# Kernel optimization log

Measured on AMD Instinct MI355X. Metric: run time of the kernel, lower is better.

Reference implementation:

```python
import jax, jax.numpy as jnp
import numpy as np

N, DIN, D, H, L, S, E = 3072, 64, 128, 4, 2, 4, 49152
NEG = -2.0**32 + 1.0


def _layernorm(x, g, b, eps=1e-5):
    m = jnp.mean(x, axis=-1, keepdims=True)
    v = jnp.var(x, axis=-1, keepdims=True)
    return (x - m) * jax.lax.rsqrt(v + eps) * g + b


def setup_inputs() -> dict:
    key = jax.random.key(0)
    ks = jax.random.split(key, 24)
    w = lambda k, shp: (0.02 * jax.random.normal(k, shp)).astype(jnp.float32)
    inp = {
        "x": jax.random.normal(ks[0], (N, DIN), dtype=jnp.float32),
        "edge_index": jax.random.randint(ks[1], (2, E), 0, N, dtype=jnp.int64) if jax.config.jax_enable_x64 else jax.random.randint(ks[1], (2, E), 0, N).astype(jnp.int32),
        "shortest_path_len": jax.random.randint(ks[2], (N, N), 0, 11).astype(jnp.int32),
        "edge_feat": jax.random.normal(ks[3], (N, N, S), dtype=jnp.float32),
        # input projection
        "node_W": w(ks[4], (DIN, D)), "node_b": jnp.zeros((D,), jnp.float32),
        # centrality / spatial / edge encodings
        "deg_emb": w(ks[5], (N, D)),
        "sp_emb": w(ks[6], (11, 1)),
        "edge_W": w(ks[7], (S, S)), "edge_b": jnp.zeros((S,), jnp.float32),
        # per-layer stacked attention params
        "ln1_g": jnp.ones((L, D), jnp.float32), "ln1_b": jnp.zeros((L, D), jnp.float32),
        "Wq": w(ks[8], (L, H, D, D)), "bq": jnp.zeros((L, H, D), jnp.float32),
        "Wk": w(ks[9], (L, H, D, D)), "bk": jnp.zeros((L, H, D), jnp.float32),
        "Wv": w(ks[10], (L, H, D, D)), "bv": jnp.zeros((L, H, D), jnp.float32),
        "Wo": w(ks[11], (L, H * D, D)), "bo": jnp.zeros((L, D), jnp.float32),
        "ln2_g": jnp.ones((L, D), jnp.float32), "ln2_b": jnp.zeros((L, D), jnp.float32),
        "ff_W": w(ks[12], (L, D, D)), "ff_b": jnp.zeros((L, D), jnp.float32),
        # output projection
        "out_W": w(ks[13], (D, D)), "out_b": jnp.zeros((D,), jnp.float32),
    }
    return inp


def reference(x, edge_index, shortest_path_len, edge_feat,
              node_W, node_b, deg_emb, sp_emb, edge_W, edge_b,
              ln1_g, ln1_b, Wq, bq, Wk, bk, Wv, bv, Wo, bo,
              ln2_g, ln2_b, ff_W, ff_b, out_W, out_b):
    # padding mask from raw features
    mask_idx = (jnp.sum(x, axis=1) != 0).astype(x.dtype)            # [N]
    mask = mask_idx[:, None] * mask_idx[None, :]                    # [N,N]

    h = x @ node_W + node_b                                         # [N,D]
    # centrality: degree of edge destinations
    deg = jax.ops.segment_sum(jnp.ones((edge_index.shape[1],), jnp.int32),
                              edge_index[1], num_segments=N)        # [N]
    h = h + deg_emb[deg]

    spatial = sp_emb[shortest_path_len][..., 0]                     # [N,N]
    edge_m = (edge_feat @ edge_W + edge_b).mean(axis=-1)            # [N,N]
    bias = spatial + edge_m
    scale = 1.0 / jnp.sqrt(jnp.asarray(D, x.dtype))

    for l in range(L):
        x_ln = _layernorm(h, ln1_g[l], ln1_b[l])                    # [N,D]
        q = jnp.einsum('nd,hdk->hnk', x_ln, Wq[l]) + bq[l][:, None, :]
        k = jnp.einsum('nd,hdk->hnk', x_ln, Wk[l]) + bk[l][:, None, :]
        v = jnp.einsum('nd,hdk->hnk', x_ln, Wv[l]) + bv[l][:, None, :]
        a = jnp.einsum('hnk,hmk->hnm', q, k) * scale + bias[None]   # [H,N,N]
        a = jnp.where(mask[None] == 0, NEG, a)
        s = jax.nn.softmax(a, axis=-1)
        s = jnp.where(mask[None] == 0, 0.0, s)
        o = jnp.einsum('hnm,hmd->hnd', s, v)                        # [H,N,D]
        cat = jnp.transpose(o, (1, 0, 2)).reshape(N, H * D)         # [N,H*D]
        x_out = cat @ Wo[l] + bo[l] + h
        h = _layernorm(x_out, ln2_g[l], ln2_b[l]) @ ff_W[l] + ff_b[l] + x_out

    return h @ out_W + out_b
```

## Files before the change

### kernel.cpp

```cpp
#include <hip/hip_runtime.h>
#include <math.h>

static constexpr int N   = 3072;
static constexpr int DIN = 64;
static constexpr int D   = 128;
static constexpr int H   = 4;
static constexpr int E   = 49152;
#define NEGV  (-4294967295.0f)
#define SCALE (0.08838834764831845f)

typedef unsigned short u16;
typedef __attribute__((ext_vector_type(8))) short short8;
typedef __attribute__((ext_vector_type(4))) float f32x4;
typedef __attribute__((ext_vector_type(4))) unsigned short u16x4;

__device__ __forceinline__ u16 f2bf(float f){
  unsigned int u = __float_as_uint(f);
  u += 0x7fff + ((u >> 16) & 1);
  return (u16)(u >> 16);
}
__device__ __forceinline__ float bf2f(u16 u){
  return __uint_as_float(((unsigned int)u) << 16);
}

// ... 30 lines not shown
    a0 = fmaf(xu, nodeW[u*D + t],      a0);
    a1 = fmaf(xu, nodeW[u*D + t + 64], a1);
  }
  h[i*D + t]      = a0;
  h[i*D + t + 64] = a1;
  float s2 = a0 + a1, sq = a0*a0 + a1*a1;
  #pragma unroll
  for(int o=32;o;o>>=1){ s2 += __shfl_xor(s2, o); sq += __shfl_xor(sq, o); }
  float mean = s2*(1.0f/128.0f);
  float var  = sq*(1.0f/128.0f) - mean*mean;
  float inv  = rsqrtf(var + 1e-5f);
  xln[i*D + t]      = (a0 - mean)*inv*g1[t]      + b1[t];
  xln[i*D + t + 64] = (a1 - mean)*inv*g1[t + 64] + b1[t + 64];
}

__global__ void k_bias(const int* __restrict__ spl, const float* __restrict__ ef,
                       const float* __restrict__ spe, const float* __restrict__ eW,
                       const float* __restrict__ eb, const float* __restrict__ mask,
                       u16* __restrict__ biasm){
  int idx = blockIdx.x*blockDim.x + threadIdx.x;
  int i = idx / N, j = idx % N;
  float wm0 = (eW[0] + eW[1] + eW[2] + eW[3])  * 0.25f;
  float wm1 = (eW[4] + eW[5] + eW[6] + eW[7])  * 0.25f;
  float wm2 = (eW[8] + eW[9] + eW[10]+ eW[11]) * 0.25f;
  float wm3 = (eW[12]+ eW[13]+ eW[14]+ eW[15]) * 0.25f;
  float bm  = (eb[0] + eb[1] + eb[2] + eb[3])  * 0.25f;
  float4 e4 = reinterpret_cast<const float4*>(ef)[idx];
  float em = fmaf(e4.x, wm0, fmaf(e4.y, wm1, fmaf(e4.z, wm2, fmaf(e4.w, wm3, bm))));
  float b = spe[spl[idx]] + em;
  float mk = mask[i]*mask[j];
  biasm[idx] = f2bf((mk != 0.0f) ? b : NEGV);
}

__global__ __launch_bounds__(256) void k_wt_all(const float* __restrict__ Wq, const float* __restrict__ Wk,
    const float* __restrict__ Wv, const float* __restrict__ ffW, const float* __restrict__ outW,
    u16* __restrict__ wt_qkv, u16* __restrict__ wt_ff, u16* __restrict__ wt_out){
  __shared__ float t[32][33];
  const int z = blockIdx.y;
  const float* src; u16* dst;
  if(z < 24){
    int l = z/12, r = z%12;
    const float* W = (r>>2)==0 ? Wq : (r>>2)==1 ? Wk : Wv;
    src = W + (size_t)(l*4 + (r&3))*16384;
    dst = wt_qkv + (size_t)z*16384;
  } else if(z < 26){
    src = ffW + (size_t)(z-24)*16384; dst = wt_ff + (size_t)(z-24)*16384;
  } else { src = outW; dst = wt_out; }
  const int ki = blockIdx.x & 3, ni = blockIdx.x >> 2;
  const int tid = threadIdx.x;
  #pragma unroll
  for(int i=0;i<4;i++){
    int idx = tid + i*256, r = idx>>5, c = idx&31;
    t[r][c] = src[(size_t)(ki*32+r)*128 + ni*32 + c];
  }
  __syncthreads();
  #pragma unroll
  for(int i=0;i<4;i++){
    int idx = tid + i*256, r = idx>>5, c = idx&31;
    dst[(size_t)(ni*32+r)*128 + ki*32 + c] = f2bf(t[c][r]);
  }
}

__global__ __launch_bounds__(256) void k_wt_wo(const float* __restrict__ Wo, u16* __restrict__ wt_wo){
  __shared__ float t[32][33];
  const int l = blockIdx.y;
  const float* src = Wo + (size_t)l*65536;
  u16* dst = wt_wo + (size_t)l*65536;
  const int ki = blockIdx.x & 15, ni = blockIdx.x >> 4;
  const int tid = threadIdx.x;
  #pragma unroll
  for(int i=0;i<4;i++){
    int idx = tid + i*256, r = idx>>5, c = idx&31;
    t[r][c] = src[(size_t)(ki*32+r)*128 + ni*32 + c];
  }
  __syncthreads();
  #pragma unroll
  for(int i=0;i<4;i++){
    int idx = tid + i*256, r = idx>>5, c = idx&31;
    dst[(size_t)(ni*32+r)*512 + ki*32 + c] = f2bf(t[c][r]);
  }
}

template<int MODE>
__device__ __forceinline__ void mgemm_body(const float* __restrict__ A, const u16* __restrict__ Bt,
                                           const float* __restrict__ bias, void* __restrict__ Cv){
  __shared__ u16 As[64*128];
  __shared__ u16 Bs[128*128];
  const int tid = threadIdx.x, w = tid>>6, lane = tid&63;
  const int g4 = lane>>4, l16 = lane&15;
  const int m0 = blockIdx.x*64;
  const int srow = tid>>4, sch = tid&15;
  f32x4 acc[8];
  #pragma unroll
  for(int nt=0;nt<8;++nt) acc[nt] = (f32x4){0.f,0.f,0.f,0.f};
  #pragma unroll
  for(int it=0;it<4;++it){
    int row = it*16 + srow;
    const float4* ap = reinterpret_cast<const float4*>(A + (size_t)(m0+row)*128 + sch*8);
    float4 x0 = ap[0], x1 = ap[1];
    u16x4 p0, p1;
    p0.x=f2bf(x0.x); p0.y=f2bf(x0.y); p0.z=f2bf(x0.z); p0.w=f2bf(x0.w);
    p1.x=f2bf(x1.x); p1.y=f2bf(x1.y); p1.z=f2bf(x1.z); p1.w=f2bf(x1.w);
    u16* dst = &As[row*128 + ((sch ^ (row&15))*8)];
    *reinterpret_cast<u16x4*>(dst)     = p0;
    *reinterpret_cast<u16x4*>(dst + 4) = p1;
  }
  #pragma unroll
  for(int it=0;it<8;++it){
    int row = it*16 + srow;
    short8 b = *reinterpret_cast<const short8*>(Bt + (size_t)row*128 + sch*8);
    *reinterpret_cast<short8*>(&Bs[row*128 + ((sch ^ (row&15))*8)]) = b;
  }
  __syncthreads();
  __builtin_amdgcn_s_setprio(1);
  #pragma unroll
  for(int c=0;c<4;++c){
    short8 af = *reinterpret_cast<const short8*>(&As[(w*16+l16)*128 + (((c*4+g4) ^ l16)*8)]);
    #pragma unroll
    for(int nt=0;nt<8;++nt){
      short8 bf = *reinterpret_cast<const short8*>(&Bs[(nt*16+l16)*128 + (((c*4+g4) ^ l16)*8)]);
      acc[nt] = __builtin_amdgcn_mfma_f32_16x16x32_bf16(af, bf, acc[nt], 0, 0, 0);
    }
  }
  __builtin_amdgcn_s_setprio(0);
  const int mrow = m0 + w*16 + g4*4;
  if(MODE == 2){
    __syncthreads();
    u16* T = Bs;
    #pragma unroll
    for(int nt=0;nt<8;++nt){
      const int col = nt*16 + l16;
      float bi = bias[col];
      u16x4 t;
      t.x = f2bf(acc[nt][0] + bi); t.y = f2bf(acc[nt][1] + bi);
      t.z = f2bf(acc[nt][2] + bi); t.w = f2bf(acc[nt][3] + bi);
      *reinterpret_cast<u16x4*>(&T[col*68 + (w*16 + g4*4)]) = t;
    }
    __syncthreads();
    #pragma unroll
    for(int i=0;i<4;++i){
      int slot = tid + i*256;
      int col = slot >> 3, q = slot & 7;
      short8 v = *reinterpret_cast<const short8*>(&T[col*68 + q*8]);
      *reinterpret_cast<short8*>((u16*)Cv + (size_t)col*N + m0 + q*8) = v;
    }
  } else {
    #pragma unroll
    for(int nt=0;nt<8;++nt){
      const int col = nt*16 + l16;
      float bi = bias[col];
      #pragma unroll
      for(int rg=0;rg<4;++rg){
        float v = acc[nt][rg] + bi;
        if(MODE == 1) ((u16*)Cv)[(size_t)(mrow+rg)*128 + col] = f2bf(v);
        else          ((float*)Cv)[(size_t)(mrow+rg)*128 + col] = v;
      }
    }
  }
}

__global__ __launch_bounds__(256) void k_mqkv(const float* __restrict__ xln, const u16* __restrict__ wt_qkv,
    const float* __restrict__ bq, const float* __restrict__ bk, const float* __restrict__ bv,
    u16* __restrict__ q, u16* __restrict__ k, u16* __restrict__ vT, int l){
  const int z = blockIdx.y, which = z>>2, head = z&3;
  const u16* Bt = wt_qkv + (size_t)(l*12 + z)*16384;
  if(which == 0)      mgemm_body<1>(xln, Bt, bq + (l*H+head)*D, q  + (size_t)head*N*D);
  else if(which == 1) mgemm_body<1>(xln, Bt, bk + (l*H+head)*D, k  + (size_t)head*N*D);
  else                mgemm_body<2>(xln, Bt, bv + (l*H+head)*D, vT + (size_t)head*N*D);
}

__global__ __launch_bounds__(256) void k_mout(const float* __restrict__ h, const u16* __restrict__ wt_out,
    const float* __restrict__ outb, float* __restrict__ out){
  mgemm_body<0>(h, wt_out, outb, out);
}

template<int S>
__global__ __launch_bounds__(256) void k_mwo(const float* __restrict__ opart, const float* __restrict__ mpart,
    const float* __restrict__ lpart, const float* __restrict__ mask, const u16* __restrict__ wt,
    const float* __restrict__ bo, const float* __restrict__ hres,
    float* __restrict__ xout, float* __restrict__ xln,
    const float* __restrict__ g2, const float* __restrict__ b2){
  __shared__ u16 As[64*128];
  __shared__ u16 Bs[128*128];
  const int tid = threadIdx.x, w = tid>>6, lane = tid&63;
  const int g4 = lane>>4, l16 = lane&15;
  const int m0 = blockIdx.x*64;
  const int srow = tid>>4, sch = tid&15;
  f32x4 acc[8];
  #pragma unroll
  for(int nt=0;nt<8;++nt) acc[nt] = (f32x4){0.f,0.f,0.f,0.f};
  for(int k0 = 0; k0 < 512; k0 += 128){
    const int hh = k0 >> 7;
    __syncthreads();
    #pragma unroll
    for(int it=0;it<4;++it){
      int row = it*16 + srow;
      int grow = m0 + row;
      float w_[S]; float M = -INFINITY; float mv[S], lv[S];
      #pragma unroll
      for(int s=0;s<S;++s){
        mv[s] = mpart[(size_t)(s*H + hh)*N + grow];
        lv[s] = lpart[(size_t)(s*H + hh)*N + grow];
        M = fmaxf(M, mv[s]);
      }
      float denom = 0.f;
      #pragma unroll
      for(int s=0;s<S;++s){ w_[s] = __expf(mv[s] - M); denom = fmaf(lv[s], w_[s], denom); }
      float scale = mask[grow] / denom;
      const int d = sch*8;
      float4 v0 = make_float4(0,0,0,0), v1 = make_float4(0,0,0,0);
      #pragma unroll
      for(int s=0;s<S;++s){
        const float4* op = reinterpret_cast<const float4*>(
            opart + ((size_t)(s*H + hh)*N + grow)*D + d);
        float4 a = op[0], b = op[1];
        v0.x = fmaf(a.x, w_[s], v0.x); v0.y = fmaf(a.y, w_[s], v0.y);
        v0.z = fmaf(a.z, w_[s], v0.z); v0.w = fmaf(a.w, w_[s], v0.w);
        v1.x = fmaf(b.x, w_[s], v1.x); v1.y = fmaf(b.y, w_[s], v1.y);
        v1.z = fmaf(b.z, w_[s], v1.z); v1.w = fmaf(b.w, w_[s], v1.w);
      }
      u16x4 p0, p1;
      p0.x=f2bf(v0.x*scale); p0.y=f2bf(v0.y*scale); p0.z=f2bf(v0.z*scale); p0.w=f2bf(v0.w*scale);
      p1.x=f2bf(v1.x*scale); p1.y=f2bf(v1.y*scale); p1.z=f2bf(v1.z*scale); p1.w=f2bf(v1.w*scale);
      u16* dst = &As[row*128 + ((sch ^ (row&15))*8)];
      *reinterpret_cast<u16x4*>(dst)     = p0;
      *reinterpret_cast<u16x4*>(dst + 4) = p1;
    }
    #pragma unroll
    for(int it=0;it<8;++it){
      int row = it*16 + srow;
      short8 b = *reinterpret_cast<const short8*>(wt + (size_t)row*512 + k0 + sch*8);
      *reinterpret_cast<short8*>(&Bs[row*128 + ((sch ^ (row&15))*8)]) = b;
    }
    __syncthreads();
    __builtin_amdgcn_s_setprio(1);
    #pragma unroll
    for(int c=0;c<4;++c){
      short8 af = *reinterpret_cast<const short8*>(&As[(w*16+l16)*128 + (((c*4+g4) ^ l16)*8)]);
      #pragma unroll
      for(int nt=0;nt<8;++nt){
        short8 bf = *reinterpret_cast<const short8*>(&Bs[(nt*16+l16)*128 + (((c*4+g4) ^ l16)*8)]);
        acc[nt] = __builtin_amdgcn_mfma_f32_16x16x32_bf16(af, bf, acc[nt], 0, 0, 0);
      }
    }
    __builtin_amdgcn_s_setprio(0);
  }
  const int mrow = m0 + w*16 + g4*4;
  float s_[4] = {0,0,0,0}, q_[4] = {0,0,0,0};
  #pragma unroll
  for(int nt=0;nt<8;++nt){
    const int col = nt*16 + l16;
    float bi = bo[col];
    #pragma unroll
    for(int rg=0;rg<4;++rg){
      float v = acc[nt][rg] + bi + hres[(size_t)(mrow+rg)*128 + col];
      acc[nt][rg] = v;
      s_[rg] += v; q_[rg] = fmaf(v, v, q_[rg]);
    }
  }
  #pragma unroll
  for(int o=1;o<16;o<<=1){
    #pragma unroll
    for(int rg=0;rg<4;++rg){ s_[rg] += __shfl_xor(s_[rg], o); q_[rg] += __shfl_xor(q_[rg], o); }
  }
  float mean[4], inv[4];
  #pragma unroll
  for(int rg=0;rg<4;++rg){
    mean[rg] = s_[rg]*(1.0f/128.0f);
    float var = q_[rg]*(1.0f/128.0f) - mean[rg]*mean[rg];
    inv[rg] = rsqrtf(var + 1e-5f);
  }
  #pragma unroll
  for(int nt=0;nt<8;++nt){
    const int col = nt*16 + l16;
    float gg = g2[col], bb = b2[col];
    #pragma unroll
    for(int rg=0;rg<4;++rg){
      float v = acc[nt][rg];
      xout[(size_t)(mrow+rg)*128 + col] = v;
      xln [(size_t)(mrow+rg)*128 + col] = (v - mean[rg])*inv[rg]*gg + bb;
    }
  }
}

__global__ __launch_bounds__(256) void k_mff(const float* __restrict__ xlnin, const u16* __restrict__ wt,
    const float* __restrict__ ffb, const float* __restrict__ res, float* __restrict__ hout,
    float* __restrict__ xlnout, const float* __restrict__ g1n, const float* __restrict__ b1n,
    int write_ln){
  __shared__ u16 As[64*128];
  __shared__ u16 Bs[128*128];
  const int tid = threadIdx.x, w = tid>>6, lane = tid&63;
  const int g4 = lane>>4, l16 = lane&15;
  const int m0 = blockIdx.x*64;
  const int srow = tid>>4, sch = tid&15;
  f32x4 acc[8];
  #pragma unroll
  for(int nt=0;nt<8;++nt) acc[nt] = (f32x4){0.f,0.f,0.f,0.f};
  #pragma unroll
  for(int it=0;it<4;++it){
    int row = it*16 + srow;
    const float4* ap = reinterpret_cast<const float4*>(xlnin + (size_t)(m0+row)*128 + sch*8);
    float4 x0 = ap[0], x1 = ap[1];
    u16x4 p0, p1;
    p0.x=f2bf(x0.x); p0.y=f2bf(x0.y); p0.z=f2bf(x0.z); p0.w=f2bf(x0.w);
    p1.x=f2bf(x1.x); p1.y=f2bf(x1.y); p1.z=f2bf(x1.z); p1.w=f2bf(x1.w);
    u16* dst = &As[row*128 + ((sch ^ (row&15))*8)];
    *reinterpret_cast<u16x4*>(dst)     = p0;
    *reinterpret_cast<u16x4*>(dst + 4) = p1;
  }
  #pragma unroll
  for(int it=0;it<8;++it){
    int row = it*16 + srow;
    short8 b = *reinterpret_cast<const short8*>(wt + (size_t)row*128 + sch*8);
    *reinterpret_cast<short8*>(&Bs[row*128 + ((sch ^ (row&15))*8)]) = b;
  }
  __syncthreads();
  __builtin_amdgcn_s_setprio(1);
  #pragma unroll
  for(int c=0;c<4;++c){
    short8 af = *reinterpret_cast<const short8*>(&As[(w*16+l16)*128 + (((c*4+g4) ^ l16)*8)]);
    #pragma unroll
    for(int nt=0;nt<8;++nt){
      short8 bf = *reinterpret_cast<const short8*>(&Bs[(nt*16+l16)*128 + (((c*4+g4) ^ l16)*8)]);
      acc[nt] = __builtin_amdgcn_mfma_f32_16x16x32_bf16(af, bf, acc[nt], 0, 0, 0);
    }
  }
  __builtin_amdgcn_s_setprio(0);
  const int mrow = m0 + w*16 + g4*4;
  float s_[4] = {0,0,0,0}, q_[4] = {0,0,0,0};
  #pragma unroll
  for(int nt=0;nt<8;++nt){
    const int col = nt*16 + l16;
    float bi = ffb[col];
    #pragma unroll
    for(int rg=0;rg<4;++rg){
      float v = acc[nt][rg] + bi + res[(size_t)(mrow+rg)*128 + col];
      acc[nt][rg] = v;
      s_[rg] += v; q_[rg] = fmaf(v, v, q_[rg]);
    }
  }
  #pragma unroll
  for(int nt=0;nt<8;++nt){
    const int col = nt*16 + l16;
    #pragma unroll
    for(int rg=0;rg<4;++rg)
      hout[(size_t)(mrow+rg)*128 + col] = acc[nt][rg];
  }
  if(write_ln){
    #pragma unroll
    for(int o=1;o<16;o<<=1){
      #pragma unroll
      for(int rg=0;rg<4;++rg){ s_[rg] += __shfl_xor(s_[rg], o); q_[rg] += __shfl_xor(q_[rg], o); }
    }
    #pragma unroll
    for(int rg=0;rg<4;++rg){
      float mean = s_[rg]*(1.0f/128.0f);
      float var  = q_[rg]*(1.0f/128.0f) - mean*mean;
      float inv  = rsqrtf(var + 1e-5f);
      s_[rg] = mean; q_[rg] = inv;
    }
    #pragma unroll
    for(int nt=0;nt<8;++nt){
      const int col = nt*16 + l16;
      float gg = g1n[col], bb = b1n[col];
      #pragma unroll
      for(int rg=0;rg<4;++rg)
        xlnout[(size_t)(mrow+rg)*128 + col] = (acc[nt][rg] - s_[rg])*q_[rg]*gg + bb;
    }
  }
}

__global__ __launch_bounds__(256) void k_attn(const u16* __restrict__ q, const u16* __restrict__ k,
                     const u16* __restrict__ vT, const u16* __restrict__ biasm,
                     float* __restrict__ opart, float* __restrict__ mpart, float* __restrict__ lpart,
                     int kvlen){
  const int tid  = threadIdx.x;
  const int w    = tid >> 6;
  const int lane = tid & 63;
  const int g4 = lane >> 4, l16 = lane & 15;
  const int head = blockIdx.y, sp = blockIdx.z;
  const int r0 = blockIdx.x*64 + w*16;
  __shared__ u16 Ks[64*128];
  __shared__ u16 Vs[64*128];
  __shared__ u16 P[4][16][40];

  const u16* qbase = q + ((size_t)head*N + r0)*D;
  short8 qf[4];
  #pragma unroll
  for(int c=0;c<4;c++)
    qf[c] = *reinterpret_cast<const short8*>(qbase + l16*D + c*32 + g4*8);

  f32x4 o[8];
  #pragma unroll
  for(int dt=0;dt<8;dt++) o[dt] = (f32x4){0.f,0.f,0.f,0.f};
  float m = -INFINITY, lsum = 0.0f;

  const u16* kh   = k  + (size_t)head*N*D;
  const u16* vTh  = vT + (size_t)head*D*N;
  const u16* brow = biasm + (size_t)(r0 + l16)*N;
  const int kv0 = sp*kvlen;

  const int krow = tid >> 4, kch = tid & 15;
  const int vrow = tid >> 3, vch = tid & 7;

  for(int j0 = kv0; j0 < kv0 + kvlen; j0 += 64){
    short8 kreg[4], vreg[4];
    #pragma unroll
    for(int it=0; it<4; ++it)
      kreg[it] = *reinterpret_cast<const short8*>(kh + (size_t)(j0 + it*16 + krow)*D + kch*8);
    #pragma unroll
    for(int it=0; it<4; ++it)
      vreg[it] = *reinterpret_cast<const short8*>(vTh + (size_t)(it*32 + vrow)*N + j0 + vch*8);
    u16x4 bb[4];
    #pragma unroll
    for(int z=0; z<4; ++z)
      bb[z] = *reinterpret_cast<const u16x4*>(brow + j0 + z*16 + g4*4);

    __syncthreads();
    #pragma unroll
    for(int it=0; it<4; ++it){
      int row = it*16 + krow;
      *reinterpret_cast<short8*>(&Ks[row*128 + ((kch ^ (row&15))*8)]) = kreg[it];
    }
    #pragma unroll
    for(int it=0; it<4; ++it){
      int d = it*32 + vrow;
      int row = d & 63, ch = ((d>>6)<<3) | vch;
      *reinterpret_cast<short8*>(&Vs[row*128 + ((ch ^ (row&15))*8)]) = vreg[it];
    }
    __syncthreads();

    #pragma unroll
    for(int ks=0; ks<2; ++ks){
      short8 kf[8];
      const int rowA = ks*32 + l16, rowB = rowA + 16;
      #pragma unroll
      for(int c=0;c<4;c++){
        kf[c]   = *reinterpret_cast<const short8*>(&Ks[rowA*128 + (((c*4+g4) ^ l16)*8)]);
        kf[4+c] = *reinterpret_cast<const short8*>(&Ks[rowB*128 + (((c*4+g4) ^ l16)*8)]);
      }
      f32x4 sA = (f32x4){0.f,0.f,0.f,0.f}, sB = sA;
      __builtin_amdgcn_s_setprio(1);
      #pragma unroll
      for(int c=0;c<4;c++){
        sA = __builtin_amdgcn_mfma_f32_16x16x32_bf16(kf[c],   qf[c], sA, 0, 0, 0);
        sB = __builtin_amdgcn_mfma_f32_16x16x32_bf16(kf[4+c], qf[c], sB, 0, 0, 0);
      }
      __builtin_amdgcn_s_setprio(0);
      u16x4 bA = bb[2*ks], bB = bb[2*ks+1];
      sA[0] = fmaf(sA[0], SCALE, bf2f(bA.x)); sA[1] = fmaf(sA[1], SCALE, bf2f(bA.y));
      sA[2] = fmaf(sA[2], SCALE, bf2f(bA.z)); sA[3] = fmaf(sA[3], SCALE, bf2f(bA.w));
      sB[0] = fmaf(sB[0], SCALE, bf2f(bB.x)); sB[1] = fmaf(sB[1], SCALE, bf2f(bB.y));
      sB[2] = fmaf(sB[2], SCALE, bf2f(bB.z)); sB[3] = fmaf(sB[3], SCALE, bf2f(bB.w));
      float pmax = fmaxf(fmaxf(fmaxf(sA[0],sA[1]), fmaxf(sA[2],sA[3])),
                         fmaxf(fmaxf(sB[0],sB[1]), fmaxf(sB[2],sB[3])));
      pmax = fmaxf(pmax, __shfl_xor(pmax, 16));
      pmax = fmaxf(pmax, __shfl_xor(pmax, 32));
      if(!__all(pmax - m <= 8.0f)){
        float mnew = fmaxf(m, pmax);
        float corr = __expf(m - mnew);
        lsum *= corr;
        float c0 = __shfl(corr, (lane & 48) | (g4*4 + 0));
        float c1 = __shfl(corr, (lane & 48) | (g4*4 + 1));
        float c2 = __shfl(corr, (lane & 48) | (g4*4 + 2));
        float c3 = __shfl(corr, (lane & 48) | (g4*4 + 3));
        #pragma unroll
        for(int dt=0;dt<8;dt++){
          o[dt][0] *= c0; o[dt][1] *= c1; o[dt][2] *= c2; o[dt][3] *= c3;
        }
        m = mnew;
      }
      f32x4 pA, pB;
      #pragma unroll
      for(int rg=0;rg<4;rg++){ pA[rg] = __expf(sA[rg] - m); pB[rg] = __expf(sB[rg] - m); }
      float ps = (pA[0]+pA[1]) + (pA[2]+pA[3]) + ((pB[0]+pB[1]) + (pB[2]+pB[3]));
      ps += __shfl_xor(ps, 16);
      ps += __shfl_xor(ps, 32);
      lsum += ps;
      u16x4 wa, wb;
      wa.x = f2bf(pA[0]); wa.y = f2bf(pA[1]); wa.z = f2bf(pA[2]); wa.w = f2bf(pA[3]);
      wb.x = f2bf(pB[0]); wb.y = f2bf(pB[1]); wb.z = f2bf(pB[2]); wb.w = f2bf(pB[3]);
      *reinterpret_cast<u16x4*>(&P[w][l16][g4*4])      = wa;
      *reinterpret_cast<u16x4*>(&P[w][l16][16 + g4*4]) = wb;
      short8 pf = *reinterpret_cast<const short8*>(&P[w][l16][g4*8]);
      __builtin_amdgcn_s_setprio(1);
      #pragma unroll
      for(int dt=0;dt<8;dt++){
        int d = dt*16 + l16;
        int row = d & 63;
        int ch  = ((dt>>2)<<3) | (ks<<2) | g4;
        short8 vf = *reinterpret_cast<const short8*>(&Vs[row*128 + ((ch ^ l16)*8)]);
        o[dt] = __builtin_amdgcn_mfma_f32_16x16x32_bf16(pf, vf, o[dt], 0, 0, 0);
      }
      __builtin_amdgcn_s_setprio(0);
    }
  }

  float* ob = opart + ((size_t)((sp*H + head)*N) + r0)*D;
  #pragma unroll
  for(int dt=0;dt<8;dt++){
    #pragma unroll
    for(int rg=0;rg<4;rg++)
      ob[(size_t)(g4*4+rg)*D + dt*16 + l16] = o[dt][rg];
  }
  if(g4 == 0){
    mpart[(size_t)(sp*H + head)*N + r0 + l16] = m;
    lpart[(size_t)(sp*H + head)*N + r0 + l16] = lsum;
  }
}

extern "C" void kernel_launch(void* const* d_in, const int* in_sizes, int n_in,
                              void* d_out, int out_size, void* d_ws, size_t ws_size,
                              hipStream_t stream){
  const float* x      = (const float*)d_in[0];
  const int*   ei     = (const int*)  d_in[1];
  const int*   spl    = (const int*)  d_in[2];
  const float* ef     = (const float*)d_in[3];
  const float* nodeW  = (const float*)d_in[4];
  const float* nodeb  = (const float*)d_in[5];
  const float* degemb = (const float*)d_in[6];
  const float* spe    = (const float*)d_in[7];
  const float* eW     = (const float*)d_in[8];
  const float* eb     = (const float*)d_in[9];
  const float* ln1g   = (const float*)d_in[10];
  const float* ln1b   = (const float*)d_in[11];
  const float* Wq     = (const float*)d_in[12];
  const float* bq     = (const float*)d_in[13];
  const float* Wk     = (const float*)d_in[14];
  const float* bk     = (const float*)d_in[15];
  const float* Wv     = (const float*)d_in[16];
  const float* bv     = (const float*)d_in[17];
  const float* Wo     = (const float*)d_in[18];
  const float* bo     = (const float*)d_in[19];
  const float* ln2g   = (const float*)d_in[20];
  const float* ln2b   = (const float*)d_in[21];
  const float* ffW    = (const float*)d_in[22];
  const float* ffb    = (const float*)d_in[23];
  const float* outW   = (const float*)d_in[24];
  const float* outb   = (const float*)d_in[25];

  constexpr size_t WT_ELEMS = 24*16384 + 2*16384 + 16384 + 2*65536;
  auto needed = [](int s)->size_t{
    size_t fl = 8192 + 3*(size_t)N*D;
    size_t bf = 3*(size_t)H*N*D + (size_t)N*N;
    size_t pf = (size_t)s*H*N*D + 2*(size_t)s*H*N;
    return fl*4 + bf*2 + pf*4 + WT_ELEMS*2;
  };
  int S = 2;
  if(needed(4) <= ws_size) S = 4;

  float* ws   = (float*)d_ws;
  int*   deg  = (int*)ws;
  float* mask = ws + 4096;
  float* h    = ws + 8192;
  float* xln  = h    + N*D;
  float* xout = xln  + N*D;
  u16*   qb   = (u16*)(xout + N*D);
  u16*   kb   = qb + (size_t)H*N*D;
  u16*   vTb  = kb + (size_t)H*N*D;
  u16*   biasm= vTb + (size_t)H*N*D;
  float* opart= (float*)(biasm + (size_t)N*N);
  float* mpart= opart + (size_t)S*H*N*D;
  float* lpart= mpart + (size_t)S*H*N;
  u16*   wt_qkv = (u16*)(lpart + (size_t)S*H*N);
  u16*   wt_ff  = wt_qkv + 24*16384;
  u16*   wt_out = wt_ff  + 2*16384;
  u16*   wt_wo  = wt_out + 16384;

  k_wt_all<<<dim3(16, 27), 256, 0, stream>>>(Wq, Wk, Wv, ffW, outW, wt_qkv, wt_ff, wt_out);
  k_wt_wo<<<dim3(64, 2), 256, 0, stream>>>(Wo, wt_wo);
  k_zero_deg<<<(N+255)/256, 256, 0, stream>>>(deg);
  k_deg<<<(E+255)/256, 256, 0, stream>>>(ei, deg);
  k_h0<<<N, 64, 0, stream>>>(x, nodeW, nodeb, degemb, deg, ln1g, ln1b, mask, h, xln);
  k_bias<<<(N*N)/256, 256, 0, stream>>>(spl, ef, spe, eW, eb, mask, biasm);

  for(int l = 0; l < 2; ++l){
    k_mqkv<<<dim3(N/64, 12), 256, 0, stream>>>(xln, wt_qkv, bq, bk, bv, qb, kb, vTb, l);
    k_attn<<<dim3(N/64, H, S), 256, 0, stream>>>(qb, kb, vTb, biasm, opart, mpart, lpart, N/S);
    if(S == 4)
      k_mwo<4><<<N/64, 256, 0, stream>>>(opart, mpart, lpart, mask, wt_wo + (size_t)l*65536,
                                         bo + l*D, h, xout, xln, ln2g + l*D, ln2b + l*D);
    else
      k_mwo<2><<<N/64, 256, 0, stream>>>(opart, mpart, lpart, mask, wt_wo + (size_t)l*65536,
                                         bo + l*D, h, xout, xln, ln2g + l*D, ln2b + l*D);
    k_mff<<<N/64, 256, 0, stream>>>(xln, wt_ff + (size_t)l*16384, ffb + l*D, xout, h, xln,
                                    ln1g + (l==0 ? D : 0), ln1b + (l==0 ? D : 0), l==0 ? 1 : 0);
  }
  k_mout<<<N/64, 256, 0, stream>>>(h, wt_out, outb, (float*)d_out);
}
```

Before: 242.3 us.

## Process two query tiles per wave in attention and raise KV split to eight

```diff
diff --git a/kernel.cpp b/kernel.cpp
--- a/kernel.cpp
+++ b/kernel.cpp
@@ -433,25 +433,29 @@
   const int lane = tid & 63;
   const int g4 = lane >> 4, l16 = lane & 15;
   const int head = blockIdx.y, sp = blockIdx.z;
-  const int r0 = blockIdx.x*64 + w*16;
+  const int r0 = blockIdx.x*128 + w*32;
   __shared__ u16 Ks[64*128];
   __shared__ u16 Vs[64*128];
-  __shared__ u16 P[4][16][40];
+  __shared__ u16 P[4][2][16][40];
 
   const u16* qbase = q + ((size_t)head*N + r0)*D;
-  short8 qf[4];
-  #pragma unroll
-  for(int c=0;c<4;c++)
-    qf[c] = *reinterpret_cast<const short8*>(qbase + l16*D + c*32 + g4*8);
-
-  f32x4 o[8];
-  #pragma unroll
-  for(int dt=0;dt<8;dt++) o[dt] = (f32x4){0.f,0.f,0.f,0.f};
-  float m = -INFINITY, lsum = 0.0f;
+  short8 qf0[4], qf1[4];
+  #pragma unroll
+  for(int c=0;c<4;c++){
+    qf0[c] = *reinterpret_cast<const short8*>(qbase + l16*D + c*32 + g4*8);
+    qf1[c] = *reinterpret_cast<const short8*>(qbase + (16+l16)*D + c*32 + g4*8);
+  }
+
+  f32x4 o0[8], o1[8];
+  #pragma unroll
+  for(int dt=0;dt<8;dt++){ o0[dt] = (f32x4){0.f,0.f,0.f,0.f}; o1[dt] = o0[dt]; }
+  float m0v = -INFINITY, ls0 = 0.0f;
+  float m1v = -INFINITY, ls1 = 0.0f;
 
   const u16* kh   = k  + (size_t)head*N*D;
   const u16* vTh  = vT + (size_t)head*D*N;
-  const u16* brow = biasm + (size_t)(r0 + l16)*N;
+  const u16* brow0 = biasm + (size_t)(r0 + l16)*N;
+  const u16* brow1 = biasm + (size_t)(r0 + 16 + l16)*N;
   const int kv0 = sp*kvlen;
 
   const int krow = tid >> 4, kch = tid & 15;
@@ -465,10 +469,12 @@
     #pragma unroll
     for(int it=0; it<4; ++it)
       vreg[it] = *reinterpret_cast<const short8*>(vTh + (size_t)(it*32 + vrow)*N + j0 + vch*8);
-    u16x4 bb[4];
-    #pragma unroll
-    for(int z=0; z<4; ++z)
-      bb[z] = *reinterpret_cast<const u16x4*>(brow + j0 + z*16 + g4*4);
+    u16x4 bb0[4], bb1[4];
+    #pragma unroll
+    for(int z=0; z<4; ++z){
+      bb0[z] = *reinterpret_cast<const u16x4*>(brow0 + j0 + z*16 + g4*4);
+      bb1[z] = *reinterpret_cast<const u16x4*>(brow1 + j0 + z*16 + g4*4);
+    }
 
     __syncthreads();
     #pragma unroll
@@ -493,50 +499,72 @@
         kf[c]   = *reinterpret_cast<const short8*>(&Ks[rowA*128 + (((c*4+g4) ^ l16)*8)]);
         kf[4+c] = *reinterpret_cast<const short8*>(&Ks[rowB*128 + (((c*4+g4) ^ l16)*8)]);
       }
-      f32x4 sA = (f32x4){0.f,0.f,0.f,0.f}, sB = sA;
+      f32x4 sA0 = (f32x4){0.f,0.f,0.f,0.f}, sB0 = sA0, sA1 = sA0, sB1 = sA0;
       __builtin_amdgcn_s_setprio(1);
       #pragma unroll
       for(int c=0;c<4;c++){
-        sA = __builtin_amdgcn_mfma_f32_16x16x32_bf16(kf[c],   qf[c], sA, 0, 0, 0);
-        sB = __builtin_amdgcn_mfma_f32_16x16x32_bf16(kf[4+c], qf[c], sB, 0, 0, 0);
+        sA0 = __builtin_amdgcn_mfma_f32_16x16x32_bf16(kf[c],   qf0[c], sA0, 0, 0, 0);
+        sB0 = __builtin_amdgcn_mfma_f32_16x16x32_bf16(kf[4+c], qf0[c], sB0, 0, 0, 0);
+        sA1 = __builtin_amdgcn_mfma_f32_16x16x32_bf16(kf[c],   qf1[c], sA1, 0, 0, 0);
+        sB1 = __builtin_amdgcn_mfma_f32_16x16x32_bf16(kf[4+c], qf1[c], sB1, 0, 0, 0);
       }
       __builtin_amdgcn_s_setprio(0);
-      u16x4 bA = bb[2*ks], bB = bb[2*ks+1];
-      sA[0] = fmaf(sA[0], SCALE, bf2f(bA.x)); sA[1] = fmaf(sA[1], SCALE, bf2f(bA.y));
-      sA[2] = fmaf(sA[2], SCALE, bf2f(bA.z)); sA[3] = fmaf(sA[3], SCALE, bf2f(bA.w));
-      sB[0] = fmaf(sB[0], SCALE, bf2f(bB.x)); sB[1] = fmaf(sB[1], SCALE, bf2f(bB.y));
-      sB[2] = fmaf(sB[2], SCALE, bf2f(bB.z)); sB[3] = fmaf(sB[3], SCALE, bf2f(bB.w));
-      float pmax = fmaxf(fmaxf(fmaxf(sA[0],sA[1]), fmaxf(sA[2],sA[3])),
-                         fmaxf(fmaxf(sB[0],sB[1]), fmaxf(sB[2],sB[3])));
-      pmax = fmaxf(pmax, __shfl_xor(pmax, 16));
-      pmax = fmaxf(pmax, __shfl_xor(pmax, 32));
-      if(!__all(pmax - m <= 8.0f)){
-        float mnew = fmaxf(m, pmax);
-        float corr = __expf(m - mnew);
-        lsum *= corr;
-        float c0 = __shfl(corr, (lane & 48) | (g4*4 + 0));
-        float c1 = __shfl(corr, (lane & 48) | (g4*4 + 1));
-        float c2 = __shfl(corr, (lane & 48) | (g4*4 + 2));
-        float c3 = __shfl(corr, (lane & 48) | (g4*4 + 3));
+      {
+        u16x4 bA = bb0[2*ks], bB = bb0[2*ks+1];
+        sA0[0] = fmaf(sA0[0], SCALE, bf2f(bA.x)); sA0[1] = fmaf(sA0[1], SCALE, bf2f(bA.y));
+        sA0[2] = fmaf(sA0[2], SCALE, bf2f(bA.z)); sA0[3] = fmaf(sA0[3], SCALE, bf2f(bA.w));
+        sB0[0] = fmaf(sB0[0], SCALE, bf2f(bB.x)); sB0[1] = fmaf(sB0[1], SCALE, bf2f(bB.y));
+        sB0[2] = fmaf(sB0[2], SCALE, bf2f(bB.z)); sB0[3] = fmaf(sB0[3], SCALE, bf2f(bB.w));
+      }
+      {
+        u16x4 bA = bb1[2*ks], bB = bb1[2*ks+1];
+        sA1[0] = fmaf(sA1[0], SCALE, bf2f(bA.x)); sA1[1] = fmaf(sA1[1], SCALE, bf2f(bA.y));
+        sA1[2] = fmaf(sA1[2], SCALE, bf2f(bA.z)); sA1[3] = fmaf(sA1[3], SCALE, bf2f(bA.w));
+        sB1[0] = fmaf(sB1[0], SCALE, bf2f(bB.x)); sB1[1] = fmaf(sB1[1], SCALE, bf2f(bB.y));
+        sB1[2] = fmaf(sB1[2], SCALE, bf2f(bB.z)); sB1[3] = fmaf(sB1[3], SCALE, bf2f(bB.w));
+      }
+      float p0 = fmaxf(fmaxf(fmaxf(sA0[0],sA0[1]), fmaxf(sA0[2],sA0[3])),
+                       fmaxf(fmaxf(sB0[0],sB0[1]), fmaxf(sB0[2],sB0[3])));
+      float p1 = fmaxf(fmaxf(fmaxf(sA1[0],sA1[1]), fmaxf(sA1[2],sA1[3])),
+                       fmaxf(fmaxf(sB1[0],sB1[1]), fmaxf(sB1[2],sB1[3])));
+      p0 = fmaxf(p0, __shfl_xor(p0, 16)); p0 = fmaxf(p0, __shfl_xor(p0, 32));
+      p1 = fmaxf(p1, __shfl_xor(p1, 16)); p1 = fmaxf(p1, __shfl_xor(p1, 32));
+      float dm = fmaxf(p0 - m0v, p1 - m1v);
+      if(!__all(dm <= 8.0f)){
+        float mn0 = fmaxf(m0v, p0), mn1 = fmaxf(m1v, p1);
+        float cr0 = __expf(m0v - mn0), cr1 = __expf(m1v - mn1);
+        ls0 *= cr0; ls1 *= cr1;
         #pragma unroll
-        for(int dt=0;dt<8;dt++){
-          o[dt][0] *= c0; o[dt][1] *= c1; o[dt][2] *= c2; o[dt][3] *= c3;
+        for(int rg=0;rg<4;++rg){
+          float c0 = __shfl(cr0, (lane & 48) | (g4*4 + rg));
+          float c1 = __shfl(cr1, (lane & 48) | (g4*4 + rg));
+          #pragma unroll
+          for(int dt=0;dt<8;dt++){ o0[dt][rg] *= c0; o1[dt][rg] *= c1; }
         }
-        m = mnew;
-      }
-      f32x4 pA, pB;
-      #pragma unroll
-      for(int rg=0;rg<4;rg++){ pA[rg] = __expf(sA[rg] - m); pB[rg] = __expf(sB[rg] - m); }
-      float ps = (pA[0]+pA[1]) + (pA[2]+pA[3]) + ((pB[0]+pB[1]) + (pB[2]+pB[3]));
-      ps += __shfl_xor(ps, 16);
-      ps += __shfl_xor(ps, 32);
-      lsum += ps;
+        m0v = mn0; m1v = mn1;
+      }
+      f32x4 pA0, pB0, pA1, pB1;
+      #pragma unroll
+      for(int rg=0;rg<4;rg++){
+        pA0[rg] = __expf(sA0[rg] - m0v); pB0[rg] = __expf(sB0[rg] - m0v);
+        pA1[rg] = __expf(sA1[rg] - m1v); pB1[rg] = __expf(sB1[rg] - m1v);
+      }
+      float ps0 = (pA0[0]+pA0[1]) + (pA0[2]+pA0[3]) + ((pB0[0]+pB0[1]) + (pB0[2]+pB0[3]));
+      float ps1 = (pA1[0]+pA1[1]) + (pA1[2]+pA1[3]) + ((pB1[0]+pB1[1]) + (pB1[2]+pB1[3]));
+      ps0 += __shfl_xor(ps0, 16); ps0 += __shfl_xor(ps0, 32);
+      ps1 += __shfl_xor(ps1, 16); ps1 += __shfl_xor(ps1, 32);
+      ls0 += ps0; ls1 += ps1;
       u16x4 wa, wb;
-      wa.x = f2bf(pA[0]); wa.y = f2bf(pA[1]); wa.z = f2bf(pA[2]); wa.w = f2bf(pA[3]);
-      wb.x = f2bf(pB[0]); wb.y = f2bf(pB[1]); wb.z = f2bf(pB[2]); wb.w = f2bf(pB[3]);
-      *reinterpret_cast<u16x4*>(&P[w][l16][g4*4])      = wa;
-      *reinterpret_cast<u16x4*>(&P[w][l16][16 + g4*4]) = wb;
-      short8 pf = *reinterpret_cast<const short8*>(&P[w][l16][g4*8]);
+      wa.x = f2bf(pA0[0]); wa.y = f2bf(pA0[1]); wa.z = f2bf(pA0[2]); wa.w = f2bf(pA0[3]);
+      wb.x = f2bf(pB0[0]); wb.y = f2bf(pB0[1]); wb.z = f2bf(pB0[2]); wb.w = f2bf(pB0[3]);
+      *reinterpret_cast<u16x4*>(&P[w][0][l16][g4*4])      = wa;
+      *reinterpret_cast<u16x4*>(&P[w][0][l16][16 + g4*4]) = wb;
+      wa.x = f2bf(pA1[0]); wa.y = f2bf(pA1[1]); wa.z = f2bf(pA1[2]); wa.w = f2bf(pA1[3]);
+      wb.x = f2bf(pB1[0]); wb.y = f2bf(pB1[1]); wb.z = f2bf(pB1[2]); wb.w = f2bf(pB1[3]);
+      *reinterpret_cast<u16x4*>(&P[w][1][l16][g4*4])      = wa;
+      *reinterpret_cast<u16x4*>(&P[w][1][l16][16 + g4*4]) = wb;
+      short8 pf0 = *reinterpret_cast<const short8*>(&P[w][0][l16][g4*8]);
+      short8 pf1 = *reinterpret_cast<const short8*>(&P[w][1][l16][g4*8]);
       __builtin_amdgcn_s_setprio(1);
       #pragma unroll
       for(int dt=0;dt<8;dt++){
@@ -544,22 +572,28 @@
         int row = d & 63;
         int ch  = ((dt>>2)<<3) | (ks<<2) | g4;
         short8 vf = *reinterpret_cast<const short8*>(&Vs[row*128 + ((ch ^ l16)*8)]);
-        o[dt] = __builtin_amdgcn_mfma_f32_16x16x32_bf16(pf, vf, o[dt], 0, 0, 0);
+        o0[dt] = __builtin_amdgcn_mfma_f32_16x16x32_bf16(pf0, vf, o0[dt], 0, 0, 0);
+        o1[dt] = __builtin_amdgcn_mfma_f32_16x16x32_bf16(pf1, vf, o1[dt], 0, 0, 0);
       }
       __builtin_amdgcn_s_setprio(0);
     }
   }
 
-  float* ob = opart + ((size_t)((sp*H + head)*N) + r0)*D;
+  float* ob0 = opart + ((size_t)((sp*H + head)*N) + r0)*D;
+  float* ob1 = ob0 + (size_t)16*D;
   #pragma unroll
   for(int dt=0;dt<8;dt++){
     #pragma unroll
-    for(int rg=0;rg<4;rg++)
-      ob[(size_t)(g4*4+rg)*D + dt*16 + l16] = o[dt][rg];
+    for(int rg=0;rg<4;rg++){
+      ob0[(size_t)(g4*4+rg)*D + dt*16 + l16] = o0[dt][rg];
+      ob1[(size_t)(g4*4+rg)*D + dt*16 + l16] = o1[dt][rg];
+    }
   }
   if(g4 == 0){
-    mpart[(size_t)(sp*H + head)*N + r0 + l16] = m;
-    lpart[(size_t)(sp*H + head)*N + r0 + l16] = lsum;
+    mpart[(size_t)(sp*H + head)*N + r0 + l16]      = m0v;
+    lpart[(size_t)(sp*H + head)*N + r0 + l16]      = ls0;
+    mpart[(size_t)(sp*H + head)*N + r0 + 16 + l16] = m1v;
+    lpart[(size_t)(sp*H + head)*N + r0 + 16 + l16] = ls1;
   }
 }
 
@@ -601,7 +635,8 @@
     return fl*4 + bf*2 + pf*4 + WT_ELEMS*2;
   };
   int S = 2;
-  if(needed(4) <= ws_size) S = 4;
+  if(needed(8) <= ws_size) S = 8;
+  else if(needed(4) <= ws_size) S = 4;
 
   float* ws   = (float*)d_ws;
   int*   deg  = (int*)ws;
@@ -630,8 +665,11 @@
 
   for(int l = 0; l < 2; ++l){
     k_mqkv<<<dim3(N/64, 12), 256, 0, stream>>>(xln, wt_qkv, bq, bk, bv, qb, kb, vTb, l);
-    k_attn<<<dim3(N/64, H, S), 256, 0, stream>>>(qb, kb, vTb, biasm, opart, mpart, lpart, N/S);
-    if(S == 4)
+    k_attn<<<dim3(N/128, H, S), 256, 0, stream>>>(qb, kb, vTb, biasm, opart, mpart, lpart, N/S);
+    if(S == 8)
+      k_mwo<8><<<N/64, 256, 0, stream>>>(opart, mpart, lpart, mask, wt_wo + (size_t)l*65536,
+                                         bo + l*D, h, xout, xln, ln2g + l*D, ln2b + l*D);
+    else if(S == 4)
       k_mwo<4><<<N/64, 256, 0, stream>>>(opart, mpart, lpart, mask, wt_wo + (size_t)l*65536,
                                          bo + l*D, h, xout, xln, ln2g + l*D, ln2b + l*D);
     else
```

Result: slower. 272.8 us (+12.6%).

## Fuse Wo, FF and output GEMMs; store attention partials in bf16

Applied to the files above, without the earlier changes.

```diff
diff --git a/kernel.cpp b/kernel.cpp
--- a/kernel.cpp
+++ b/kernel.cpp
@@ -206,8 +206,7 @@
       #pragma unroll
       for(int rg=0;rg<4;++rg){
         float v = acc[nt][rg] + bi;
-        if(MODE == 1) ((u16*)Cv)[(size_t)(mrow+rg)*128 + col] = f2bf(v);
-        else          ((float*)Cv)[(size_t)(mrow+rg)*128 + col] = v;
+        ((u16*)Cv)[(size_t)(mrow+rg)*128 + col] = f2bf(v);
       }
     }
   }
@@ -223,17 +222,16 @@
   else                mgemm_body<2>(xln, Bt, bv + (l*H+head)*D, vT + (size_t)head*N*D);
 }
 
-__global__ __launch_bounds__(256) void k_mout(const float* __restrict__ h, const u16* __restrict__ wt_out,
-    const float* __restrict__ outb, float* __restrict__ out){
-  mgemm_body<0>(h, wt_out, outb, out);
-}
-
-template<int S>
-__global__ __launch_bounds__(256) void k_mwo(const float* __restrict__ opart, const float* __restrict__ mpart,
-    const float* __restrict__ lpart, const float* __restrict__ mask, const u16* __restrict__ wt,
-    const float* __restrict__ bo, const float* __restrict__ hres,
-    float* __restrict__ xout, float* __restrict__ xln,
-    const float* __restrict__ g2, const float* __restrict__ b2){
+template<int S, bool LAST>
+__global__ __launch_bounds__(256) void k_mwoff(const u16* __restrict__ opart, const float* __restrict__ mpart,
+    const float* __restrict__ lpart, const float* __restrict__ mask, const u16* __restrict__ wt_wo_l,
+    const float* __restrict__ bo_l, const float* __restrict__ hres,
+    const u16* __restrict__ wt_ff_l, const float* __restrict__ ffb_l,
+    const float* __restrict__ g2, const float* __restrict__ b2,
+    float* __restrict__ hout, float* __restrict__ xlnout,
+    const float* __restrict__ g1n, const float* __restrict__ b1n,
+    const u16* __restrict__ wt_out_m, const float* __restrict__ outb_m,
+    float* __restrict__ finalout){
   __shared__ u16 As[64*128];
   __shared__ u16 Bs[128*128];
   const int tid = threadIdx.x, w = tid>>6, lane = tid&63;
@@ -262,20 +260,17 @@
       for(int s=0;s<S;++s){ w_[s] = __expf(mv[s] - M); denom = fmaf(lv[s], w_[s], denom); }
       float scale = mask[grow] / denom;
       const int d = sch*8;
-      float4 v0 = make_float4(0,0,0,0), v1 = make_float4(0,0,0,0);
+      float v[8] = {0,0,0,0,0,0,0,0};
       #pragma unroll
       for(int s=0;s<S;++s){
-        const float4* op = reinterpret_cast<const float4*>(
+        short8 ov = *reinterpret_cast<const short8*>(
             opart + ((size_t)(s*H + hh)*N + grow)*D + d);
-        float4 a = op[0], b = op[1];
-        v0.x = fmaf(a.x, w_[s], v0.x); v0.y = fmaf(a.y, w_[s], v0.y);
-        v0.z = fmaf(a.z, w_[s], v0.z); v0.w = fmaf(a.w, w_[s], v0.w);
-        v1.x = fmaf(b.x, w_[s], v1.x); v1.y = fmaf(b.y, w_[s], v1.y);
-        v1.z = fmaf(b.z, w_[s], v1.z); v1.w = fmaf(b.w, w_[s], v1.w);
+        #pragma unroll
+        for(int j=0;j<8;++j) v[j] = fmaf(bf2f((u16)ov[j]), w_[s], v[j]);
       }
       u16x4 p0, p1;
-      p0.x=f2bf(v0.x*scale); p0.y=f2bf(v0.y*scale); p0.z=f2bf(v0.z*scale); p0.w=f2bf(v0.w*scale);
-      p1.x=f2bf(v1.x*scale); p1.y=f2bf(v1.y*scale); p1.z=f2bf(v1.z*scale); p1.w=f2bf(v1.w*scale);
+      p0.x=f2bf(v[0]*scale); p0.y=f2bf(v[1]*scale); p0.z=f2bf(v[2]*scale); p0.w=f2bf(v[3]*scale);
+      p1.x=f2bf(v[4]*scale); p1.y=f2bf(v[5]*scale); p1.z=f2bf(v[6]*scale); p1.w=f2bf(v[7]*scale);
       u16* dst = &As[row*128 + ((sch ^ (row&15))*8)];
       *reinterpret_cast<u16x4*>(dst)     = p0;
       *reinterpret_cast<u16x4*>(dst + 4) = p1;
@@ -283,7 +278,7 @@
     #pragma unroll
     for(int it=0;it<8;++it){
       int row = it*16 + srow;
-      short8 b = *reinterpret_cast<const short8*>(wt + (size_t)row*512 + k0 + sch*8);
+      short8 b = *reinterpret_cast<const short8*>(wt_wo_l + (size_t)row*512 + k0 + sch*8);
       *reinterpret_cast<short8*>(&Bs[row*128 + ((sch ^ (row&15))*8)]) = b;
     }
     __syncthreads();
@@ -304,7 +299,7 @@
   #pragma unroll
   for(int nt=0;nt<8;++nt){
     const int col = nt*16 + l16;
-    float bi = bo[col];
+    float bi = bo_l[col];
     #pragma unroll
     for(int rg=0;rg<4;++rg){
       float v = acc[nt][rg] + bi + hres[(size_t)(mrow+rg)*128 + col];
@@ -324,51 +319,28 @@
     float var = q_[rg]*(1.0f/128.0f) - mean[rg]*mean[rg];
     inv[rg] = rsqrtf(var + 1e-5f);
   }
+  __syncthreads();
   #pragma unroll
   for(int nt=0;nt<8;++nt){
     const int col = nt*16 + l16;
+    const int ch = col >> 3, wi = col & 7;
     float gg = g2[col], bb = b2[col];
     #pragma unroll
     for(int rg=0;rg<4;++rg){
-      float v = acc[nt][rg];
-      xout[(size_t)(mrow+rg)*128 + col] = v;
-      xln [(size_t)(mrow+rg)*128 + col] = (v - mean[rg])*inv[rg]*gg + bb;
-    }
-  }
-}
-
-__global__ __launch_bounds__(256) void k_mff(const float* __restrict__ xlnin, const u16* __restrict__ wt,
-    const float* __restrict__ ffb, const float* __restrict__ res, float* __restrict__ hout,
-    float* __restrict__ xlnout, const float* __restrict__ g1n, const float* __restrict__ b1n,
-    int write_ln){
-  __shared__ u16 As[64*128];
-  __shared__ u16 Bs[128*128];
-  const int tid = threadIdx.x, w = tid>>6, lane = tid&63;
-  const int g4 = lane>>4, l16 = lane&15;
-  const int m0 = blockIdx.x*64;
-  const int srow = tid>>4, sch = tid&15;
-  f32x4 acc[8];
-  #pragma unroll
-  for(int nt=0;nt<8;++nt) acc[nt] = (f32x4){0.f,0.f,0.f,0.f};
-  #pragma unroll
-  for(int it=0;it<4;++it){
-    int row = it*16 + srow;
-    const float4* ap = reinterpret_cast<const float4*>(xlnin + (size_t)(m0+row)*128 + sch*8);
-    float4 x0 = ap[0], x1 = ap[1];
-    u16x4 p0, p1;
-    p0.x=f2bf(x0.x); p0.y=f2bf(x0.y); p0.z=f2bf(x0.z); p0.w=f2bf(x0.w);
-    p1.x=f2bf(x1.x); p1.y=f2bf(x1.y); p1.z=f2bf(x1.z); p1.w=f2bf(x1.w);
-    u16* dst = &As[row*128 + ((sch ^ (row&15))*8)];
-    *reinterpret_cast<u16x4*>(dst)     = p0;
-    *reinterpret_cast<u16x4*>(dst + 4) = p1;
+      int row = w*16 + g4*4 + rg;
+      As[row*128 + ((ch ^ (row&15))*8) + wi] = f2bf((acc[nt][rg] - mean[rg])*inv[rg]*gg + bb);
+    }
   }
   #pragma unroll
   for(int it=0;it<8;++it){
     int row = it*16 + srow;
-    short8 b = *reinterpret_cast<const short8*>(wt + (size_t)row*128 + sch*8);
+    short8 b = *reinterpret_cast<const short8*>(wt_ff_l + (size_t)row*128 + sch*8);
     *reinterpret_cast<short8*>(&Bs[row*128 + ((sch ^ (row&15))*8)]) = b;
   }
   __syncthreads();
+  f32x4 acc2[8];
+  #pragma unroll
+  for(int nt=0;nt<8;++nt) acc2[nt] = (f32x4){0.f,0.f,0.f,0.f};
   __builtin_amdgcn_s_setprio(1);
   #pragma unroll
   for(int c=0;c<4;++c){
@@ -376,42 +348,40 @@
     #pragma unroll
     for(int nt=0;nt<8;++nt){
       short8 bf = *reinterpret_cast<const short8*>(&Bs[(nt*16+l16)*128 + (((c*4+g4) ^ l16)*8)]);
-      acc[nt] = __builtin_amdgcn_mfma_f32_16x16x32_bf16(af, bf, acc[nt], 0, 0, 0);
+      acc2[nt] = __builtin_amdgcn_mfma_f32_16x16x32_bf16(af, bf, acc2[nt], 0, 0, 0);
     }
   }
   __builtin_amdgcn_s_setprio(0);
-  const int mrow = m0 + w*16 + g4*4;
-  float s_[4] = {0,0,0,0}, q_[4] = {0,0,0,0};
   #pragma unroll
   for(int nt=0;nt<8;++nt){
     const int col = nt*16 + l16;
-    float bi = ffb[col];
+    float bi = ffb_l[col];
+    #pragma unroll
+    for(int rg=0;rg<4;++rg)
+      acc2[nt][rg] += bi + acc[nt][rg];
+  }
+  if(!LAST){
+    float s2_[4] = {0,0,0,0}, q2_[4] = {0,0,0,0};
+    #pragma unroll
+    for(int nt=0;nt<8;++nt){
+      const int col = nt*16 + l16;
+      #pragma unroll
+      for(int rg=0;rg<4;++rg){
+        float v = acc2[nt][rg];
+        hout[(size_t)(mrow+rg)*128 + col] = v;
+        s2_[rg] += v; q2_[rg] = fmaf(v, v, q2_[rg]);
+      }
+    }
+    #pragma unroll
+    for(int o=1;o<16;o<<=1){
+      #pragma unroll
+      for(int rg=0;rg<4;++rg){ s2_[rg] += __shfl_xor(s2_[rg], o); q2_[rg] += __shfl_xor(q2_[rg], o); }
+    }
     #pragma unroll
     for(int rg=0;rg<4;++rg){
-      float v = acc[nt][rg] + bi + res[(size_t)(mrow+rg)*128 + col];
-      acc[nt][rg] = v;
-      s_[rg] += v; q_[rg] = fmaf(v, v, q_[rg]);
-    }
-  }
-  #pragma unroll
-  for(int nt=0;nt<8;++nt){
-    const int col = nt*16 + l16;
-    #pragma unroll
-    for(int rg=0;rg<4;++rg)
-      hout[(size_t)(mrow+rg)*128 + col] = acc[nt][rg];
-  }
-  if(write_ln){
-    #pragma unroll
-    for(int o=1;o<16;o<<=1){
-      #pragma unroll
-      for(int rg=0;rg<4;++rg){ s_[rg] += __shfl_xor(s_[rg], o); q_[rg] += __shfl_xor(q_[rg], o); }
-    }
-    #pragma unroll
-    for(int rg=0;rg<4;++rg){
-      float mean = s_[rg]*(1.0f/128.0f);
-      float var  = q_[rg]*(1.0f/128.0f) - mean*mean;
-      float inv  = rsqrtf(var + 1e-5f);
-      s_[rg] = mean; q_[rg] = inv;
+      float mn = s2_[rg]*(1.0f/128.0f);
+      float var = q2_[rg]*(1.0f/128.0f) - mn*mn;
+      s2_[rg] = mn; q2_[rg] = rsqrtf(var + 1e-5f);
     }
     #pragma unroll
     for(int nt=0;nt<8;++nt){
@@ -419,14 +389,55 @@
       float gg = g1n[col], bb = b1n[col];
       #pragma unroll
       for(int rg=0;rg<4;++rg)
-        xlnout[(size_t)(mrow+rg)*128 + col] = (acc[nt][rg] - s_[rg])*q_[rg]*gg + bb;
+        xlnout[(size_t)(mrow+rg)*128 + col] = (acc2[nt][rg] - s2_[rg])*q2_[rg]*gg + bb;
+    }
+  } else {
+    __syncthreads();
+    #pragma unroll
+    for(int nt=0;nt<8;++nt){
+      const int col = nt*16 + l16;
+      const int ch = col >> 3, wi = col & 7;
+      #pragma unroll
+      for(int rg=0;rg<4;++rg){
+        int row = w*16 + g4*4 + rg;
+        As[row*128 + ((ch ^ (row&15))*8) + wi] = f2bf(acc2[nt][rg]);
+      }
+    }
+    #pragma unroll
+    for(int it=0;it<8;++it){
+      int row = it*16 + srow;
+      short8 b = *reinterpret_cast<const short8*>(wt_out_m + (size_t)row*128 + sch*8);
+      *reinterpret_cast<short8*>(&Bs[row*128 + ((sch ^ (row&15))*8)]) = b;
+    }
+    __syncthreads();
+    f32x4 acc3[8];
+    #pragma unroll
+    for(int nt=0;nt<8;++nt) acc3[nt] = (f32x4){0.f,0.f,0.f,0.f};
+    __builtin_amdgcn_s_setprio(1);
+    #pragma unroll
+    for(int c=0;c<4;++c){
+      short8 af = *reinterpret_cast<const short8*>(&As[(w*16+l16)*128 + (((c*4+g4) ^ l16)*8)]);
+      #pragma unroll
+      for(int nt=0;nt<8;++nt){
+        short8 bf = *reinterpret_cast<const short8*>(&Bs[(nt*16+l16)*128 + (((c*4+g4) ^ l16)*8)]);
+        acc3[nt] = __builtin_amdgcn_mfma_f32_16x16x32_bf16(af, bf, acc3[nt], 0, 0, 0);
+      }
+    }
+    __builtin_amdgcn_s_setprio(0);
+    #pragma unroll
+    for(int nt=0;nt<8;++nt){
+      const int col = nt*16 + l16;
+      float bi = outb_m[col];
+      #pragma unroll
+      for(int rg=0;rg<4;++rg)
+        finalout[(size_t)(mrow+rg)*128 + col] = acc3[nt][rg] + bi;
     }
   }
 }
 
 __global__ __launch_bounds__(256) void k_attn(const u16* __restrict__ q, const u16* __restrict__ k,
                      const u16* __restrict__ vT, const u16* __restrict__ biasm,
-                     float* __restrict__ opart, float* __restrict__ mpart, float* __restrict__ lpart,
+                     u16* __restrict__ opart, float* __restrict__ mpart, float* __restrict__ lpart,
                      int kvlen){
   const int tid  = threadIdx.x;
   const int w    = tid >> 6;
@@ -550,12 +561,12 @@
     }
   }
 
-  float* ob = opart + ((size_t)((sp*H + head)*N) + r0)*D;
+  u16* ob = opart + ((size_t)((sp*H + head)*N) + r0)*D;
   #pragma unroll
   for(int dt=0;dt<8;dt++){
     #pragma unroll
     for(int rg=0;rg<4;rg++)
-      ob[(size_t)(g4*4+rg)*D + dt*16 + l16] = o[dt][rg];
+      ob[(size_t)(g4*4+rg)*D + dt*16 + l16] = f2bf(o[dt][rg]);
   }
   if(g4 == 0){
     mpart[(size_t)(sp*H + head)*N + r0 + l16] = m;
@@ -596,12 +607,13 @@
   constexpr size_t WT_ELEMS = 24*16384 + 2*16384 + 16384 + 2*65536;
   auto needed = [](int s)->size_t{
     size_t fl = 8192 + 3*(size_t)N*D;
-    size_t bf = 3*(size_t)H*N*D + (size_t)N*N;
-    size_t pf = (size_t)s*H*N*D + 2*(size_t)s*H*N;
+    size_t bf = 3*(size_t)H*N*D + (size_t)N*N + (size_t)s*H*N*D;
+    size_t pf = 2*(size_t)s*H*N;
     return fl*4 + bf*2 + pf*4 + WT_ELEMS*2;
   };
   int S = 2;
-  if(needed(4) <= ws_size) S = 4;
+  if(needed(8) <= ws_size) S = 8;
+  else if(needed(4) <= ws_size) S = 4;
 
   float* ws   = (float*)d_ws;
   int*   deg  = (int*)ws;
@@ -613,8 +625,8 @@
   u16*   kb   = qb + (size_t)H*N*D;
   u16*   vTb  = kb + (size_t)H*N*D;
   u16*   biasm= vTb + (size_t)H*N*D;
-  float* opart= (float*)(biasm + (size_t)N*N);
-  float* mpart= opart + (size_t)S*H*N*D;
+  u16*   opart= biasm + (size_t)N*N;
+  float* mpart= (float*)(opart + (size_t)S*H*N*D);
   float* lpart= mpart + (size_t)S*H*N;
   u16*   wt_qkv = (u16*)(lpart + (size_t)S*H*N);
   u16*   wt_ff  = wt_qkv + 24*16384;
@@ -631,14 +643,34 @@
   for(int l = 0; l < 2; ++l){
     k_mqkv<<<dim3(N/64, 12), 256, 0, stream>>>(xln, wt_qkv, bq, bk, bv, qb, kb, vTb, l);
     k_attn<<<dim3(N/64, H, S), 256, 0, stream>>>(qb, kb, vTb, biasm, opart, mpart, lpart, N/S);
-    if(S == 4)
-      k_mwo<4><<<N/64, 256, 0, stream>>>(opart, mpart, lpart, mask, wt_wo + (size_t)l*65536,
-                                         bo + l*D, h, xout, xln, ln2g + l*D, ln2b + l*D);
-    else
-      k_mwo<2><<<N/64, 256, 0, stream>>>(opart, mpart, lpart, mask, wt_wo + (size_t)l*65536,
-                                         bo + l*D, h, xout, xln, ln2g + l*D, ln2b + l*D);
-    k_mff<<<N/64, 256, 0, stream>>>(xln, wt_ff + (size_t)l*16384, ffb + l*D, xout, h, xln,
-                                    ln1g + (l==0 ? D : 0), ln1b + (l==0 ? D : 0), l==0 ? 1 : 0);
-  }
-  k_mout<<<N/64, 256, 0, stream>>>(h, wt_out, outb, (float*)d_out);
-}
+    const u16* wwo = wt_wo + (size_t)l*65536;
+    const u16* wff = wt_ff + (size_t)l*16384;
+    if(l == 0){
+      if(S == 8)
+        k_mwoff<8,false><<<N/64, 256, 0, stream>>>(opart, mpart, lpart, mask, wwo, bo + l*D, h,
+            wff, ffb + l*D, ln2g + l*D, ln2b + l*D, h, xln, ln1g + D, ln1b + D,
+            nullptr, nullptr, nullptr);
+      else if(S == 4)
+        k_mwoff<4,false><<<N/64, 256, 0, stream>>>(opart, mpart, lpart, mask, wwo, bo + l*D, h,
+            wff, ffb + l*D, ln2g + l*D, ln2b + l*D, h, xln, ln1g + D, ln1b + D,
+            nullptr, nullptr, nullptr);
+      else
+        k_mwoff<2,false><<<N/64, 256, 0, stream>>>(opart, mpart, lpart, mask, wwo, bo + l*D, h,
+            wff, ffb + l*D, ln2g + l*D, ln2b + l*D, h, xln, ln1g + D, ln1b + D,
+            nullptr, nullptr, nullptr);
+    } else {
+      if(S == 8)
+        k_mwoff<8,true><<<N/64, 256, 0, stream>>>(opart, mpart, lpart, mask, wwo, bo + l*D, h,
+            wff, ffb + l*D, ln2g + l*D, ln2b + l*D, nullptr, nullptr, nullptr, nullptr,
+            wt_out, outb, (float*)d_out);
+      else if(S == 4)
+        k_mwoff<4,true><<<N/64, 256, 0, stream>>>(opart, mpart, lpart, mask, wwo, bo + l*D, h,
+            wff, ffb + l*D, ln2g + l*D, ln2b + l*D, nullptr, nullptr, nullptr, nullptr,
+            wt_out, outb, (float*)d_out);
+      else
+        k_mwoff<2,true><<<N/64, 256, 0, stream>>>(opart, mpart, lpart, mask, wwo, bo + l*D, h,
+            wff, ffb + l*D, ln2g + l*D, ln2b + l*D, nullptr, nullptr, nullptr, nullptr,
+            wt_out, outb, (float*)d_out);
+    }
+  }
+}
```

Measured after the change: 219.8 us, median of 2. 9.3% less time.
